# Kernel tuning notes

Measured on AMD Instinct MI355X. Metric: run time of the kernel, lower is better.

The kernel has to match this reference:

```python
import jax, jax.numpy as jnp
import numpy as np

N_NODES = 100000


def setup_inputs() -> dict:
    key = jax.random.key(0)
    ks = jax.random.split(key, 9)
    x = jax.random.normal(ks[0], (N_NODES, 500), dtype=jnp.float32)
    # lin1: Linear(m=500, hidden=64, bias=False) -> weight [hidden, m]
    W1 = jax.random.normal(ks[1], (64, 500), dtype=jnp.float32) * 0.02
    # lin_final: Linear(3*hidden=192, m_y=10, bias=False) -> weight [m_y, 3*hidden]
    Wf = jax.random.normal(ks[2], (10, 192), dtype=jnp.float32) * 0.02
    # 1-hop normalized adjacency in COO form (600k nnz)
    src1 = jax.random.randint(ks[3], (600000,), 0, N_NODES, dtype=jnp.int32)
    dst1 = jax.random.randint(ks[4], (600000,), 0, N_NODES, dtype=jnp.int32)
    val1 = jax.random.uniform(ks[5], (600000,), dtype=jnp.float32)
    # 2-hop normalized adjacency in COO form (1.2M nnz)
    src2 = jax.random.randint(ks[6], (1200000,), 0, N_NODES, dtype=jnp.int32)
    dst2 = jax.random.randint(ks[7], (1200000,), 0, N_NODES, dtype=jnp.int32)
    val2 = jax.random.uniform(ks[8], (1200000,), dtype=jnp.float32)
    return {"x": x, "W1": W1, "Wf": Wf,
            "src1": src1, "dst1": dst1, "val1": val1,
            "src2": src2, "dst2": dst2, "val2": val2}


def _spmm(src, dst, val, h):
    # sparse.mm(A, h): out[dst] += val * h[src]
    return jax.ops.segment_sum(val[:, None] * h[src], dst, num_segments=N_NODES)


def reference(x, W1, Wf, src1, dst1, val1, src2, dst2, val2):
    h = jax.nn.relu(x @ W1.T)                 # [N, hidden]
    h1 = _spmm(src1, dst1, val1, h)           # [N, hidden]
    h2 = _spmm(src2, dst2, val2, h)           # [N, hidden]
    h_final = jnp.concatenate([h, h1, h2], axis=1)  # [N, 3*hidden]
    # dropout is identity in eval mode
    return h_final @ Wf.T                     # [N, m_y]
```

## Files before the change

### kernel.cpp

```cpp
#include <hip/hip_runtime.h>
#include <hip/hip_bf16.h>

#define NN    100000
#define KD    500
#define KP    512
#define HID   64
#define LWS   264
#define GSP   16
#define DB    32
#define NB    3125
#define CHUNK 4096

typedef short frag8 __attribute__((ext_vector_type(8)));
typedef float f32x4 __attribute__((ext_vector_type(4)));

static __device__ __forceinline__ unsigned short f2b(float f) {
    return __builtin_bit_cast(unsigned short, __float2bfloat16(f));
}

__global__ __launch_bounds__(256) void k0_w1bf(const float* __restrict__ W1,
                                               unsigned short* __restrict__ W1bf)
{
    const int i = blockIdx.x * 256 + threadIdx.x;
    const int c = i >> 9;
    const int k = i & 511;
    const float v = (k < KD) ? W1[c * KD + k] : 0.f;
    W1bf[i] = f2b(v);
}

__global__ __launch_bounds__(256, 4) void k1_mfma(const float* __restrict__ x,
                                                  const unsigned short* __restrict__ W1bf,
                                                  float* __restrict__ h, int n)
{
    __shared__ unsigned short lw[64 * LWS];
    const int tid   = threadIdx.x;
    const int lane  = tid & 63;
    const int wid   = tid >> 6;
    const int l15   = lane & 15;
    const int l4    = lane >> 4;
    const int koffl = 8 * l4;

    const long rowBlk = (long)blockIdx.x * 64;
    long ra = rowBlk + wid * 16 + l15;
    if (ra >= n) ra = n - 1;
    const float* xp = x + ra * KD + koffl;

    f32x4 acc[4] = {};
    const float4 z = make_float4(0.f, 0.f, 0.f, 0.f);

    for (int c = 0; c < 2; ++c) {
        if (c) __syncthreads();
        #pragma unroll
        for (int it = 0; it < 8; ++it) {
            const int idx = tid + it * 256;
            const int r   = idx >> 5;
            const int q   = idx & 31;
            *(uint4*)&lw[r * LWS + q * 8] =
                *(const uint4*)&W1bf[r * KP + c * 256 + q * 8];
        }
        __syncthreads();

        int k0 = c * 256;
        float4 lo = (k0 + koffl     < KD) ? *(const float4*)(xp + k0)     : z;
        float4 hi = (k0 + koffl + 4 < KD) ? *(const float4*)(xp + k0 + 4) : z;

        #pragma unroll
        for (int ks = 0; ks < 8; ++ks) {
            float4 nlo = z, nhi = z;
            if (ks < 7) {
                const int kn = c * 256 + (ks + 1) * 32;
                nlo = (kn + koffl     < KD) ? *(const float4*)(xp + kn)     : z;
                nhi = (kn + koffl + 4 < KD) ? *(const float4*)(xp + kn + 4) : z;
            }
            frag8 a;
            a[0]=f2b(lo.x); a[1]=f2b(lo.y); a[2]=f2b(lo.z); a[3]=f2b(lo.w);
            a[4]=f2b(hi.x); a[5]=f2b(hi.y); a[6]=f2b(hi.z); a[7]=f2b(hi.w);
            const int koffw = ks * 32 + koffl;
            #pragma unroll
            for (int g = 0; g < 4; ++g) {
                const frag8 b = *(const frag8*)&lw[(g * 16 + l15) * LWS + koffw];
                acc[g] = __builtin_amdgcn_mfma_f32_16x16x32_bf16(a, b, acc[g], 0, 0, 0);
            }
            lo = nlo; hi = nhi;
        }
    }

    #pragma unroll
    for (int r = 0; r < 4; ++r) {
        const long row = rowBlk + wid * 16 + l4 * 4 + r;
        if (row < n) {
            #pragma unroll
            for (int g = 0; g < 4; ++g)
                h[row * HID + g * 16 + l15] = fmaxf(acc[g][r], 0.f);
        }
    }
}

__global__ __launch_bounds__(256) void k2_proj(const float* __restrict__ h,
                                               const float* __restrict__ Wf,
                                               float* __restrict__ out,
                                               float* __restrict__ g1,
                                               float* __restrict__ g2, int n)
{
    __shared__ float lwf[10 * 196];
    const int tid = threadIdx.x;
    for (int idx = tid; idx < 480; idx += 256) {
        const int j = idx / 48;
        const int q = idx - j * 48;
        const float4 v = *(const float4*)&Wf[j * 192 + 4 * q];
        *(float4*)&lwf[j * 196 + 4 * q] = v;
    }
    __syncthreads();

    const long row = (long)blockIdx.x * 8 + (tid >> 5);
    const int  j   = tid & 31;
    if (row < n && j < 30) {
        const int wrow = (j < 10) ? j : ((j < 20) ? j - 10 : j - 20);
        const int coff = (j < 10) ? 0 : ((j < 20) ? 64 : 128);
        const float* wp = &lwf[wrow * 196 + coff];
        const float* hp = &h[row * HID];
        float s = 0.f;
        #pragma unroll
        for (int q = 0; q < 16; ++q) {
            const float4 hv = *(const float4*)&hp[4 * q];
            const float4 wv = *(const float4*)&wp[4 * q];
            s += hv.x * wv.x + hv.y * wv.y + hv.z * wv.z + hv.w * wv.w;
        }
        if (j < 10)      out[row * 10 + j] = s;
        else if (j < 20) g1[row * GSP + (j - 10)] = s;
        else             g2[row * GSP + (j - 20)] = s;
    }
}

__global__ __launch_bounds__(256) void kA_hist(const int* __restrict__ dst1, int nnz1,
                                               const int* __restrict__ dst2, int ntE,
                                               int* __restrict__ Cmat)
{
    __shared__ int cnt[NB];
    const int tid = threadIdx.x, blk = blockIdx.x;
    for (int i = tid; i < NB; i += 256) cnt[i] = 0;
    __syncthreads();
    const int base = blk * CHUNK;
    #pragma unroll
    for (int it = 0; it < CHUNK / 256; ++it) {
        const int id = base + it * 256 + tid;
        if (id < ntE) {
            const int d = (id < nnz1) ? dst1[id] : dst2[id - nnz1];
            atomicAdd(&cnt[d / DB], 1);
        }
    }
    __syncthreads();
    for (int b = tid; b < NB; b += 256) Cmat[(size_t)blk * NB + b] = cnt[b];
}

__global__ __launch_bounds__(256) void kS1_rowscan(const int* __restrict__ Cmat, int nblk,
                                                   int* __restrict__ OFFmat,
                                                   int* __restrict__ rowSum)
{
    __shared__ int ls[256];
    const int b = blockIdx.x, tid = threadIdx.x;
    const int i0 = 2 * tid, i1 = 2 * tid + 1;
    const int e0 = (i0 < nblk) ? Cmat[(size_t)i0 * NB + b] : 0;
    const int e1 = (i1 < nblk) ? Cmat[(size_t)i1 * NB + b] : 0;
    const int ps = e0 + e1;
    ls[tid] = ps;
    __syncthreads();
    for (int off = 1; off < 256; off <<= 1) {
        const int v = (tid >= off) ? ls[tid - off] : 0;
        __syncthreads();
        ls[tid] += v;
        __syncthreads();
    }
    const int excl = ls[tid] - ps;
    if (i0 < nblk) OFFmat[(size_t)i0 * NB + b] = excl;
    if (i1 < nblk) OFFmat[(size_t)i1 * NB + b] = excl + e0;
    if (tid == 255) rowSum[b] = ls[255];
}

__global__ __launch_bounds__(256) void kS2_basescan(const int* __restrict__ rowSum,
                                                    int* __restrict__ rowBase)
{
    __shared__ int ls[256];
    const int tid = threadIdx.x;
    const int EPT = (NB + 255) / 256;
    int e[13]; int s = 0;
    #pragma unroll
    for (int u = 0; u < 13; ++u) {
        const int i = tid * EPT + u;
        e[u] = (i < NB) ? rowSum[i] : 0;
        s += e[u];
    }
    ls[tid] = s;
    __syncthreads();
    for (int off = 1; off < 256; off <<= 1) {
        const int v = (tid >= off) ? ls[tid - off] : 0;
        __syncthreads();
        ls[tid] += v;
        __syncthreads();
    }
    int run = ls[tid] - s;
    #pragma unroll
    for (int u = 0; u < 13; ++u) {
        const int i = tid * EPT + u;
        if (i < NB) rowBase[i] = run;
        run += e[u];
    }
}

__global__ __launch_bounds__(256) void kC_fill(const int* __restrict__ src1,
                                               const int* __restrict__ dst1,
                                               const float* __restrict__ val1, int nnz1,
                                               const int* __restrict__ src2,
                                               const int* __restrict__ dst2,
                                               const float* __restrict__ val2, int ntE,
                                               const int* __restrict__ OFFmat,
                                               const int* __restrict__ rowBase,
                                               uint2* __restrict__ bins)
{
    __shared__ int cur[NB];
    const int tid = threadIdx.x, blk = blockIdx.x;
    for (int b = tid; b < NB; b += 256)
        cur[b] = rowBase[b] + OFFmat[(size_t)blk * NB + b];
    __syncthreads();
    const int base = blk * CHUNK;
    #pragma unroll
    for (int it = 0; it < CHUNK / 256; ++it) {
        const int id = base + it * 256 + tid;
        if (id < ntE) {
            const bool h1 = id < nnz1;
            const int  ii = h1 ? id : id - nnz1;
            const int   s = h1 ? src1[ii] : src2[ii];
            const int   d = h1 ? dst1[ii] : dst2[ii];
            const float v = h1 ? val1[ii] : val2[ii];
            const int   b = d / DB;
            const int slot = atomicAdd(&cur[b], 1);
            uint2 r;
            r.x = (unsigned)s | ((unsigned)(!h1) << 17) | ((unsigned)(d - b * DB) << 18);
            r.y = __builtin_bit_cast(unsigned, v);
            bins[slot] = r;
        }
    }
}

__global__ __launch_bounds__(256) void kD_acc(const uint2* __restrict__ bins,
                                              const int* __restrict__ rowBase,
                                              const int* __restrict__ rowSum,
                                              const float* __restrict__ g1,
                                              const float* __restrict__ g2,
                                              float* __restrict__ out)
{
    __shared__ float lacc[DB * 10];
    const int tid = threadIdx.x, b = blockIdx.x;
    for (int i = tid; i < DB * 10; i += 256) lacc[i] = 0.f;
    __syncthreads();
    const int start = rowBase[b];
    const int nt    = rowSum[b] * 10;
    for (int i0 = tid; i0 < nt; i0 += 1024) {
        float c[4]; int li[4];
        #pragma unroll
        for (int u = 0; u < 4; ++u) {
            const int i = i0 + u * 256;
            li[u] = -1;
            c[u] = 0.f;
            if (i < nt) {
                const int e = (int)((unsigned)i / 10u);
                const int j = i - 10 * e;
                const uint2 r = bins[start + e];
                const int   src = r.x & 0x1FFFF;
                const float* gp = ((r.x >> 17) & 1) ? g2 : g1;
                c[u]  = __builtin_bit_cast(float, r.y) * gp[(size_t)src * GSP + j];
                li[u] = (int)(r.x >> 18) * 10 + j;
            }
        }
        #pragma unroll
        for (int u = 0; u < 4; ++u)
            if (li[u] >= 0) atomicAdd(&lacc[li[u]], c[u]);
    }
    __syncthreads();
    float* op = out + (size_t)b * DB * 10;
    for (int i = tid; i < DB * 10; i += 256)
        op[i] += lacc[i];
}

__global__ __launch_bounds__(256) void k_scatter_dir(const int* __restrict__ src1,
                                                     const int* __restrict__ dst1,
                                                     const float* __restrict__ val1, int n1,
                                                     const int* __restrict__ src2,
                                                     const int* __restrict__ dst2,
                                                     const float* __restrict__ val2, int nt,
                                                     const float* __restrict__ g1,
                                                     const float* __restrict__ g2,
                                                     float* __restrict__ out)
{
    const int t = blockIdx.x * 256 + threadIdx.x;
    if (t >= nt) return;
    const bool h1 = t < n1;
    const int  tt = h1 ? t : t - n1;
    const int  e  = (int)((unsigned)tt / 10u);
    const int  j  = tt - 10 * e;
    const int* sp = h1 ? src1 : src2;
    const int* dp = h1 ? dst1 : dst2;
    const float* vp = h1 ? val1 : val2;
    const float* gp = h1 ? g1 : g2;
    unsafeAtomicAdd(&out[(size_t)dp[e] * 10 + j],
                    vp[e] * gp[(size_t)sp[e] * GSP + j]);
}

extern "C" void kernel_launch(void* const* d_in, const int* in_sizes, int n_in,
                              void* d_out, int out_size, void* d_ws, size_t ws_size,
                              hipStream_t stream)
{
    const float* x    = (const float*)d_in[0];
    const float* W1   = (const float*)d_in[1];
    const float* Wf   = (const float*)d_in[2];
    const int*   src1 = (const int*)d_in[3];
    const int*   dst1 = (const int*)d_in[4];
    const float* val1 = (const float*)d_in[5];
    const int*   src2 = (const int*)d_in[6];
    const int*   dst2 = (const int*)d_in[7];
    const float* val2 = (const float*)d_in[8];
    const int nnz1 = in_sizes[3];
    const int nnz2 = in_sizes[6];
    const int ntE  = nnz1 + nnz2;
    const int n = NN;
    const int nblk = (ntE + CHUNK - 1) / CHUNK;

    char* p = (char*)d_ws;
    unsigned short* W1bf = (unsigned short*)p;       p += (size_t)64 * KP * 2;
    float* h    = (float*)p;                         p += (size_t)NN * HID * 4;
    float* g1   = (float*)p;                         p += (size_t)NN * GSP * 4;
    float* g2   = (float*)p;                         p += (size_t)NN * GSP * 4;
    uint2* bins = (uint2*)p;                         p += (size_t)ntE * 8;
    int* Cmat   = (int*)p;                           p += (size_t)NB * nblk * 4;
    int* OFFmat = (int*)p;                           p += (size_t)NB * nblk * 4;
    int* rowSum = (int*)p;                           p += (size_t)NB * 4;
    int* rowBase= (int*)p;                           p += (size_t)NB * 4;
    float* out  = (float*)d_out;
    const size_t ws_need = (size_t)(p - (char*)d_ws);

    k0_w1bf<<<128, 256, 0, stream>>>(W1, W1bf);
    k1_mfma<<<(n + 63) / 64, 256, 0, stream>>>(x, W1bf, h, n);
    k2_proj<<<(n + 7) / 8, 256, 0, stream>>>(h, Wf, out, g1, g2, n);

    if (ws_size >= ws_need) {
        kA_hist<<<nblk, 256, 0, stream>>>(dst1, nnz1, dst2, ntE, Cmat);
        kS1_rowscan<<<NB, 256, 0, stream>>>(Cmat, nblk, OFFmat, rowSum);
        kS2_basescan<<<1, 256, 0, stream>>>(rowSum, rowBase);
        kC_fill<<<nblk, 256, 0, stream>>>(src1, dst1, val1, nnz1,
                                          src2, dst2, val2, ntE,
                                          OFFmat, rowBase, bins);
        kD_acc<<<NB, 256, 0, stream>>>(bins, rowBase, rowSum, g1, g2, out);
    } else {
        const int n1 = 10 * nnz1;
        const int nt = n1 + 10 * nnz2;
        k_scatter_dir<<<(nt + 255) / 256, 256, 0, stream>>>(src1, dst1, val1, n1,
                                                            src2, dst2, val2, nt,
                                                            g1, g2, out);
    }
}
```

Measured before the change: 274.6 us.

## Pack hop projections into one fp16 buffer, serial column scan, smaller chunks

The two fp32 projected-feature buffers become a single interleaved fp16 buffer (20 values per node at stride 32), so each gathered source node touches one 64-byte row. This cuts the bytes moved in the random gather inside the accumulate kernel. The histogram chunk size is halved, the per-bin block scan is replaced by one thread per bin walking the chunks serially, and the accumulate loop is unrolled 8 ways instead of 4. The fp16 storage adds rounding error to the neighbour contributions, and the serial scan with more chunks may be slower for the scan step.

New measurement: 466.3 us. +69.8%, slower.

```diff
diff --git a/kernel.cpp b/kernel.cpp
--- a/kernel.cpp
+++ b/kernel.cpp
@@ -6,10 +6,10 @@
 #define KP    512
 #define HID   64
 #define LWS   264
-#define GSP   16
+#define GPS   32
 #define DB    32
 #define NB    3125
-#define CHUNK 4096
+#define CHUNK 2048
 
 typedef short frag8 __attribute__((ext_vector_type(8)));
 typedef float f32x4 __attribute__((ext_vector_type(4)));
@@ -99,8 +99,7 @@
 __global__ __launch_bounds__(256) void k2_proj(const float* __restrict__ h,
                                                const float* __restrict__ Wf,
                                                float* __restrict__ out,
-                                               float* __restrict__ g1,
-                                               float* __restrict__ g2, int n)
+                                               _Float16* __restrict__ gpk, int n)
 {
     __shared__ float lwf[10 * 196];
     const int tid = threadIdx.x;
@@ -127,8 +126,8 @@
             s += hv.x * wv.x + hv.y * wv.y + hv.z * wv.z + hv.w * wv.w;
         }
         if (j < 10)      out[row * 10 + j] = s;
-        else if (j < 20) g1[row * GSP + (j - 10)] = s;
-        else             g2[row * GSP + (j - 20)] = s;
+        else if (j < 20) gpk[row * GPS + (j - 10)]      = (_Float16)s;
+        else             gpk[row * GPS + 10 + (j - 20)] = (_Float16)s;
     }
 }
 
@@ -153,28 +152,19 @@
     for (int b = tid; b < NB; b += 256) Cmat[(size_t)blk * NB + b] = cnt[b];
 }
 
-__global__ __launch_bounds__(256) void kS1_rowscan(const int* __restrict__ Cmat, int nblk,
+__global__ __launch_bounds__(256) void kS1_colscan(const int* __restrict__ Cmat, int nblk,
                                                    int* __restrict__ OFFmat,
                                                    int* __restrict__ rowSum)
 {
-    __shared__ int ls[256];
-    const int b = blockIdx.x, tid = threadIdx.x;
-    const int i0 = 2 * tid, i1 = 2 * tid + 1;
-    const int e0 = (i0 < nblk) ? Cmat[(size_t)i0 * NB + b] : 0;
-    const int e1 = (i1 < nblk) ? Cmat[(size_t)i1 * NB + b] : 0;
-    const int ps = e0 + e1;
-    ls[tid] = ps;
-    __syncthreads();
-    for (int off = 1; off < 256; off <<= 1) {
-        const int v = (tid >= off) ? ls[tid - off] : 0;
-        __syncthreads();
-        ls[tid] += v;
-        __syncthreads();
-    }
-    const int excl = ls[tid] - ps;
-    if (i0 < nblk) OFFmat[(size_t)i0 * NB + b] = excl;
-    if (i1 < nblk) OFFmat[(size_t)i1 * NB + b] = excl + e0;
-    if (tid == 255) rowSum[b] = ls[255];
+    const int b = blockIdx.x * 256 + threadIdx.x;
+    if (b >= NB) return;
+    int run = 0;
+    for (int c = 0; c < nblk; ++c) {
+        const int v = Cmat[(size_t)c * NB + b];
+        OFFmat[(size_t)c * NB + b] = run;
+        run += v;
+    }
+    rowSum[b] = run;
 }
 
 __global__ __launch_bounds__(256) void kS2_basescan(const int* __restrict__ rowSum,
@@ -245,8 +235,7 @@
 __global__ __launch_bounds__(256) void kD_acc(const uint2* __restrict__ bins,
                                               const int* __restrict__ rowBase,
                                               const int* __restrict__ rowSum,
-                                              const float* __restrict__ g1,
-                                              const float* __restrict__ g2,
+                                              const _Float16* __restrict__ gpk,
                                               float* __restrict__ out)
 {
     __shared__ float lacc[DB * 10];
@@ -255,10 +244,10 @@
     __syncthreads();
     const int start = rowBase[b];
     const int nt    = rowSum[b] * 10;
-    for (int i0 = tid; i0 < nt; i0 += 1024) {
-        float c[4]; int li[4];
-        #pragma unroll
-        for (int u = 0; u < 4; ++u) {
+    for (int i0 = tid; i0 < nt; i0 += 2048) {
+        float c[8]; int li[8];
+        #pragma unroll
+        for (int u = 0; u < 8; ++u) {
             const int i = i0 + u * 256;
             li[u] = -1;
             c[u] = 0.f;
@@ -267,13 +256,14 @@
                 const int j = i - 10 * e;
                 const uint2 r = bins[start + e];
                 const int   src = r.x & 0x1FFFF;
-                const float* gp = ((r.x >> 17) & 1) ? g2 : g1;
-                c[u]  = __builtin_bit_cast(float, r.y) * gp[(size_t)src * GSP + j];
+                const int   hop = (r.x >> 17) & 1;
+                c[u]  = __builtin_bit_cast(float, r.y)
+                        * (float)gpk[(size_t)src * GPS + hop * 10 + j];
                 li[u] = (int)(r.x >> 18) * 10 + j;
             }
         }
         #pragma unroll
-        for (int u = 0; u < 4; ++u)
+        for (int u = 0; u < 8; ++u)
             if (li[u] >= 0) atomicAdd(&lacc[li[u]], c[u]);
     }
     __syncthreads();
@@ -288,8 +278,7 @@
                                                      const int* __restrict__ src2,
                                                      const int* __restrict__ dst2,
                                                      const float* __restrict__ val2, int nt,
-                                                     const float* __restrict__ g1,
-                                                     const float* __restrict__ g2,
+                                                     const _Float16* __restrict__ gpk,
                                                      float* __restrict__ out)
 {
     const int t = blockIdx.x * 256 + threadIdx.x;
@@ -301,9 +290,8 @@
     const int* sp = h1 ? src1 : src2;
     const int* dp = h1 ? dst1 : dst2;
     const float* vp = h1 ? val1 : val2;
-    const float* gp = h1 ? g1 : g2;
     unsafeAtomicAdd(&out[(size_t)dp[e] * 10 + j],
-                    vp[e] * gp[(size_t)sp[e] * GSP + j]);
+                    vp[e] * (float)gpk[(size_t)sp[e] * GPS + (h1 ? 0 : 10) + j]);
 }
 
 extern "C" void kernel_launch(void* const* d_in, const int* in_sizes, int n_in,
@@ -327,34 +315,33 @@
 
     char* p = (char*)d_ws;
     unsigned short* W1bf = (unsigned short*)p;       p += (size_t)64 * KP * 2;
-    float* h    = (float*)p;                         p += (size_t)NN * HID * 4;
-    float* g1   = (float*)p;                         p += (size_t)NN * GSP * 4;
-    float* g2   = (float*)p;                         p += (size_t)NN * GSP * 4;
-    uint2* bins = (uint2*)p;                         p += (size_t)ntE * 8;
-    int* Cmat   = (int*)p;                           p += (size_t)NB * nblk * 4;
-    int* OFFmat = (int*)p;                           p += (size_t)NB * nblk * 4;
-    int* rowSum = (int*)p;                           p += (size_t)NB * 4;
-    int* rowBase= (int*)p;                           p += (size_t)NB * 4;
-    float* out  = (float*)d_out;
+    float* h      = (float*)p;                       p += (size_t)NN * HID * 4;
+    _Float16* gpk = (_Float16*)p;                    p += (size_t)NN * GPS * 2;
+    uint2* bins   = (uint2*)p;                       p += (size_t)ntE * 8;
+    int* Cmat     = (int*)p;                         p += (size_t)NB * nblk * 4;
+    int* OFFmat   = (int*)p;                         p += (size_t)NB * nblk * 4;
+    int* rowSum   = (int*)p;                         p += (size_t)NB * 4;
+    int* rowBase  = (int*)p;                         p += (size_t)NB * 4;
+    float* out    = (float*)d_out;
     const size_t ws_need = (size_t)(p - (char*)d_ws);
 
     k0_w1bf<<<128, 256, 0, stream>>>(W1, W1bf);
     k1_mfma<<<(n + 63) / 64, 256, 0, stream>>>(x, W1bf, h, n);
-    k2_proj<<<(n + 7) / 8, 256, 0, stream>>>(h, Wf, out, g1, g2, n);
+    k2_proj<<<(n + 7) / 8, 256, 0, stream>>>(h, Wf, out, gpk, n);
 
     if (ws_size >= ws_need) {
         kA_hist<<<nblk, 256, 0, stream>>>(dst1, nnz1, dst2, ntE, Cmat);
-        kS1_rowscan<<<NB, 256, 0, stream>>>(Cmat, nblk, OFFmat, rowSum);
+        kS1_colscan<<<(NB + 255) / 256, 256, 0, stream>>>(Cmat, nblk, OFFmat, rowSum);
         kS2_basescan<<<1, 256, 0, stream>>>(rowSum, rowBase);
         kC_fill<<<nblk, 256, 0, stream>>>(src1, dst1, val1, nnz1,
                                           src2, dst2, val2, ntE,
                                           OFFmat, rowBase, bins);
-        kD_acc<<<NB, 256, 0, stream>>>(bins, rowBase, rowSum, g1, g2, out);
+        kD_acc<<<NB, 256, 0, stream>>>(bins, rowBase, rowSum, gpk, out);
     } else {
         const int n1 = 10 * nnz1;
         const int nt = n1 + 10 * nnz2;
         k_scatter_dir<<<(nt + 255) / 256, 256, 0, stream>>>(src1, dst1, val1, n1,
                                                             src2, dst2, val2, nt,
-                                                            g1, g2, out);
-    }
-}
+                                                            gpk, out);
+    }
+}
```
